# Kernel optimization log

Hardware: AMD Instinct MI355X
Metric: run time of the kernel (lower is better)

The kernel has to match this reference:

```python
import jax, jax.numpy as jnp
import numpy as np

B, N, D, H = 1, 4096, 768, 12
HD = D // H
SCALE = HD ** -0.5

def setup_inputs() -> dict:
    key = jax.random.key(0)
    k1, k2, k3 = jax.random.split(key, 3)
    x = jax.random.normal(k1, (B, N, D), dtype=jnp.float32)
    W_qkv = jax.random.normal(k2, (D, 3 * D), dtype=jnp.float32) * (D ** -0.5)
    W_out = jax.random.normal(k3, (D, D), dtype=jnp.float32) * (D ** -0.5)
    b_out = jnp.zeros((D,), dtype=jnp.float32)
    return {"x": x, "W_qkv": W_qkv, "W_out": W_out, "b_out": b_out}

def reference(x, W_qkv, W_out, b_out):
    # qkv projection: (B,N,3D)
    qkv = x @ W_qkv
    q, k, v = jnp.split(qkv, 3, axis=-1)
    # (B,N,D) -> (B,H,N,hd)
    def heads(t):
        return t.reshape(B, N, H, HD).transpose(0, 2, 1, 3)
    q, k, v = heads(q), heads(k), heads(v)
    scores = jnp.einsum('bhnd,bhmd->bhnm', q, k) * SCALE  # (B,H,N,N)
    attn = jax.nn.softmax(scores, axis=-1)
    out = jnp.einsum('bhnm,bhmd->bhnd', attn, v)
    out = out.transpose(0, 2, 1, 3).reshape(B, N, D)
    return out @ W_out + b_out
```

## Files before the change

kernel.cpp:

```cpp
#include <hip/hip_runtime.h>
#include <hip/hip_bf16.h>
#include <math.h>

typedef __attribute__((ext_vector_type(8))) short bf16x8;
typedef __attribute__((ext_vector_type(4))) float floatx4;

constexpr int kN  = 4096;
constexpr int kD  = 768;
constexpr int kH  = 12;
constexpr int kHD = 64;
constexpr int k3D = 2304;
constexpr float kQScale = 0.18033688011112042f;

static __device__ __forceinline__ short f2b(float f) {
    __hip_bfloat16 h = __float2bfloat16(f);
    return *reinterpret_cast<short*>(&h);
}

static __device__ __forceinline__ float fast_exp2(float x) {
#if __has_builtin(__builtin_amdgcn_exp2f)
    return __builtin_amdgcn_exp2f(x);
#else
    return exp2f(x);
#endif
}

static __device__ __forceinline__ void async_copy16(const void* g, void* l) {
    __builtin_amdgcn_global_load_lds(
        (const __attribute__((address_space(1))) void*)g,
        (__attribute__((address_space(3))) void*)l, 16, 0, 0);
}

__global__ __launch_bounds__(256)
void convX(const float* __restrict__ src, short* __restrict__ dst, int n8)
{
    int i = blockIdx.x * 256 + threadIdx.x;
    if (i < n8) {
        const float4* s = reinterpret_cast<const float4*>(src + (size_t)i * 8);
        float4 a = s[0], b = s[1];
        bf16x8 v;
        v[0] = f2b(a.x); v[1] = f2b(a.y); v[2] = f2b(a.z); v[3] = f2b(a.w);
        v[4] = f2b(b.x); v[5] = f2b(b.y); v[6] = f2b(b.z); v[7] = f2b(b.w);
        *reinterpret_cast<bf16x8*>(dst + (size_t)i * 8) = v;
    }
}

__global__ void convT(const float* __restrict__ src, short* __restrict__ dst,
                      int R, int C)
{
    __shared__ float t[32][33];
    const int c0 = blockIdx.x * 32, r0 = blockIdx.y * 32;
    const int tx = threadIdx.x, ty = threadIdx.y;
    #pragma unroll
    for (int i = ty; i < 32; i += 8)
        t[i][tx] = src[(size_t)(r0 + i) * C + c0 + tx];
    __syncthreads();
    #pragma unroll
    for (int i = ty; i < 32; i += 8)
        dst[(size_t)(c0 + i) * R + r0 + tx] = f2b(t[tx][i]);
}

__global__ __launch_bounds__(256)
void gemm_bt(const short* __restrict__ A, const short* __restrict__ BT,
             const float* __restrict__ bias, float* __restrict__ Cout,
             short* __restrict__ Qh, short* __restrict__ Kh, short* __restrict__ Vt,
             int N, int K, int mode)
{
    const int bm   = blockIdx.x * 128;
    const int bn   = blockIdx.y * 128;
    const int tid  = threadIdx.x;
    const int wave = tid >> 6;
    const int lane = tid & 63;
    const int l15  = lane & 15;
    const int quad = lane >> 4;
    const int l3   = l15 & 3;

    __shared__ alignas(16) short As[128 * 32];
    __shared__ alignas(16) short Bs[128 * 32];

    floatx4 acc[4][4] = {};
    const int wm = (wave >> 1) * 64;
    const int wn = (wave & 1) * 64;

    const int srl = lane >> 2;
    const int scc = (lane & 3) ^ (srl & 3);

    for (int k0 = 0; k0 < K; k0 += 32) {
        __syncthreads();
        #pragma unroll
        for (int j = 0; j < 2; ++j) {
            const int rs = 32 * wave + 16 * j;
            async_copy16(&A [(size_t)(bm + rs + srl) * K + k0 + 8 * scc], &As[rs * 32]);
            async_copy16(&BT[(size_t)(bn + rs + srl) * K + k0 + 8 * scc], &Bs[rs * 32]);
        }
        __syncthreads();

        bf16x8 af[4], bfr[4];
        #pragma unroll
        for (int mt = 0; mt < 4; ++mt)
            af[mt] = *reinterpret_cast<const bf16x8*>(&As[(wm + 16 * mt + l15) * 32 + 8 * (quad ^ l3)]);
        #pragma unroll
        for (int nt = 0; nt < 4; ++nt)
            bfr[nt] = *reinterpret_cast<const bf16x8*>(&Bs[(wn + 16 * nt + l15) * 32 + 8 * (quad ^ l3)]);
        #pragma unroll
        for (int mt = 0; mt < 4; ++mt)
            #pragma unroll
            for (int nt = 0; nt < 4; ++nt)
                acc[mt][nt] = __builtin_amdgcn_mfma_f32_16x16x32_bf16(af[mt], bfr[nt], acc[mt][nt], 0, 0, 0);
    }

    #pragma unroll
    for (int mt = 0; mt < 4; ++mt) {
        #pragma unroll
        for (int nt = 0; nt < 4; ++nt) {
            #pragma unroll
            for (int r = 0; r < 4; ++r) {
                const int row = bm + wm + mt * 16 + 4 * quad + r;
                const int col = bn + wn + nt * 16 + l15;
                float v = acc[mt][nt][r];
                if (mode == 0) {
                    Cout[(size_t)row * N + col] = v + bias[col];
                } else {
                    const int proj   = col / kD;
                    const int within = col - proj * kD;
                    const int h = within >> 6;
                    const int d = within & 63;
                    if (proj == 0)      Qh[((size_t)h * kN + row) * kHD + d] = f2b(v * kQScale);
                    else if (proj == 1) Kh[((size_t)h * kN + row) * kHD + d] = f2b(v);
                    else                Vt[((size_t)h * kHD + d) * kN + row] = f2b(v);
                }
            }
        }
    }
}

__global__ __launch_bounds__(256)
void attn(const short* __restrict__ Qh, const short* __restrict__ Kh,
          const short* __restrict__ Vt, short* __restrict__ AO)
{
    const int h    = blockIdx.y;
    const int q0   = blockIdx.x * 64;
    const int tid  = threadIdx.x;
    const int wave = tid >> 6;
    const int lane = tid & 63;
    const int l15  = lane & 15;
    const int quad = lane >> 4;
    const int lx   = l15 & 7;

    __shared__ alignas(16) short Ks[128 * 64];
    __shared__ alignas(16) short Vs[64 * 128];

    const int qrow = q0 + 16 * wave + l15;
    const size_t qbase = ((size_t)h * kN + qrow) * kHD;
    bf16x8 qf[2];
    qf[0] = *reinterpret_cast<const bf16x8*>(&Qh[qbase + quad * 8]);
    qf[1] = *reinterpret_cast<const bf16x8*>(&Qh[qbase + 32 + quad * 8]);

    floatx4 oacc[4] = {};
    float psum[4] = {0.f, 0.f, 0.f, 0.f};

    const int krl = lane >> 3;
    const int kcc = (lane & 7) ^ (krl & 7);
    const int vrl = lane >> 4;
    const int vp  = lane & 15;

    short* Pw = Ks + wave * 2048;

    for (int kv0 = 0; kv0 < kN; kv0 += 128) {
        __syncthreads();
        #pragma unroll
        for (int j = 0; j < 4; ++j) {
            const int rk = 32 * wave + 8 * j;
            async_copy16(&Kh[((size_t)h * kN + kv0 + rk + krl) * kHD + 8 * kcc],
                         &Ks[rk * 64]);
            const int rv0 = 16 * wave + 4 * j;
            const int rv  = rv0 + vrl;
            async_copy16(&Vt[((size_t)h * kHD + rv) * kN + kv0 + 8 * (vp ^ (rv & 7))],
                         &Vs[rv0 * 128]);
        }
        __syncthreads();

        floatx4 sacc[8] = {};
        #pragma unroll
        for (int nt = 0; nt < 8; ++nt) {
            #pragma unroll
            for (int s = 0; s < 2; ++s) {
                bf16x8 kf = *reinterpret_cast<const bf16x8*>(
                    &Ks[(16 * nt + l15) * 64 + 8 * ((4 * s + quad) ^ lx)]);
                sacc[nt] = __builtin_amdgcn_mfma_f32_16x16x32_bf16(qf[s], kf, sacc[nt], 0, 0, 0);
            }
        }
        __syncthreads();

        #pragma unroll
        for (int nt = 0; nt < 8; ++nt) {
            #pragma unroll
            for (int r = 0; r < 4; ++r) {
                const float p = fast_exp2(sacc[nt][r]);
                const int m = 4 * quad + r;
                Pw[m * 128 + 8 * ((2 * nt + (l15 >> 3)) ^ (m & 7)) + (l15 & 7)] = f2b(p);
                psum[r] += p;
            }
        }

        #pragma unroll
        for (int s = 0; s < 4; ++s) {
            bf16x8 pa = *reinterpret_cast<const bf16x8*>(
                &Pw[l15 * 128 + 8 * ((4 * s + quad) ^ lx)]);
            #pragma unroll
            for (int dt = 0; dt < 4; ++dt) {
                bf16x8 vv = *reinterpret_cast<const bf16x8*>(
                    &Vs[(16 * dt + l15) * 128 + 8 * ((4 * s + quad) ^ lx)]);
                oacc[dt] = __builtin_amdgcn_mfma_f32_16x16x32_bf16(pa, vv, oacc[dt], 0, 0, 0);
            }
        }
    }

    float lrow[4];
    #pragma unroll
    for (int r = 0; r < 4; ++r) {
        float v = psum[r];
        #pragma unroll
        for (int off = 8; off >= 1; off >>= 1)
            v += __shfl_xor(v, off);
        lrow[r] = v;
    }

    #pragma unroll
    for (int dt = 0; dt < 4; ++dt) {
        #pragma unroll
        for (int r = 0; r < 4; ++r) {
            const int row = q0 + 16 * wave + 4 * quad + r;
            const int col = h * kHD + 16 * dt + l15;
            AO[(size_t)row * kD + col] = f2b(oacc[dt][r] / lrow[r]);
        }
    }
}

extern "C" void kernel_launch(void* const* d_in, const int* in_sizes, int n_in,
                              void* d_out, int out_size, void* d_ws, size_t ws_size,
                              hipStream_t stream)
{
    const float* x     = (const float*)d_in[0];
    const float* W_qkv = (const float*)d_in[1];
    const float* W_out = (const float*)d_in[2];
    const float* b_out = (const float*)d_in[3];
    float* out = (float*)d_out;

    const size_t HNHD = (size_t)kH * kN * kHD;
    short* Qh    = (short*)d_ws;
    short* Kh    = Qh + HNHD;
    short* Vt    = Kh + HNHD;
    short* Xb    = Vt + HNHD;
    short* WqkvT = Xb + (size_t)kN * kD;
    short* WoutT = WqkvT + (size_t)k3D * kD;
    short* AO    = Xb;
    (void)in_sizes; (void)n_in; (void)out_size; (void)ws_size;

    convX<<<dim3((kN * kD / 8 + 255) / 256), dim3(256), 0, stream>>>(x, Xb, kN * kD / 8);
    convT<<<dim3(k3D / 32, kD / 32), dim3(32, 8), 0, stream>>>(W_qkv, WqkvT, kD, k3D);
    convT<<<dim3(kD / 32, kD / 32), dim3(32, 8), 0, stream>>>(W_out, WoutT, kD, kD);

    gemm_bt<<<dim3(kN / 128, k3D / 128), dim3(256), 0, stream>>>(
        Xb, WqkvT, nullptr, nullptr, Qh, Kh, Vt, k3D, kD, 1);
    attn<<<dim3(kN / 64, kH), dim3(256), 0, stream>>>(Qh, Kh, Vt, AO);
    gemm_bt<<<dim3(kN / 128, kD / 128), dim3(256), 0, stream>>>(
        AO, WoutT, b_out, out, nullptr, nullptr, nullptr, kD, kD, 0);
}
```

Before: 227.9 us.

## Merge prep kernels, template GEMM modes, and reswizzle attention P buffer

Folds the X conversion and both weight transposes into one prep launch, which removes two kernel launches. The GEMM mode becomes a template parameter so each specialization drops its runtime branch in the epilogue. In attention, the P tile's XOR swizzle changes from m&7 to (5*m)&15 and the write loop is reordered so the row base is computed once, aiming to cut LDS bank conflicts on the P writes and reads. The new swizzle must stay consistent between the write and read sides or the results will be wrong.

```diff
diff --git a/kernel.cpp b/kernel.cpp
--- a/kernel.cpp
+++ b/kernel.cpp
@@ -31,26 +31,38 @@
         (__attribute__((address_space(3))) void*)l, 16, 0, 0);
 }
 
-__global__ __launch_bounds__(256)
-void convX(const float* __restrict__ src, short* __restrict__ dst, int n8)
-{
-    int i = blockIdx.x * 256 + threadIdx.x;
-    if (i < n8) {
-        const float4* s = reinterpret_cast<const float4*>(src + (size_t)i * 8);
+constexpr int kBlkX  = 1536;
+constexpr int kBlkWq = 72 * 24;
+constexpr int kBlkWo = 24 * 24;
+
+__global__ __launch_bounds__(256)
+void prep(const float* __restrict__ x, const float* __restrict__ Wq,
+          const float* __restrict__ Wo, short* __restrict__ Xb,
+          short* __restrict__ WqT, short* __restrict__ WoT)
+{
+    const int bid = blockIdx.x;
+    const int tid = threadIdx.x;
+    if (bid < kBlkX) {
+        const int i = bid * 256 + tid;
+        const float4* s = reinterpret_cast<const float4*>(x + (size_t)i * 8);
         float4 a = s[0], b = s[1];
         bf16x8 v;
         v[0] = f2b(a.x); v[1] = f2b(a.y); v[2] = f2b(a.z); v[3] = f2b(a.w);
         v[4] = f2b(b.x); v[5] = f2b(b.y); v[6] = f2b(b.z); v[7] = f2b(b.w);
-        *reinterpret_cast<bf16x8*>(dst + (size_t)i * 8) = v;
-    }
-}
-
-__global__ void convT(const float* __restrict__ src, short* __restrict__ dst,
-                      int R, int C)
-{
+        *reinterpret_cast<bf16x8*>(Xb + (size_t)i * 8) = v;
+        return;
+    }
+    const float* src; short* dst; int R, C, bx, by;
+    if (bid < kBlkX + kBlkWq) {
+        const int local = bid - kBlkX;
+        src = Wq; dst = WqT; R = kD; C = k3D; bx = local % 72; by = local / 72;
+    } else {
+        const int local = bid - kBlkX - kBlkWq;
+        src = Wo; dst = WoT; R = kD; C = kD; bx = local % 24; by = local / 24;
+    }
     __shared__ float t[32][33];
-    const int c0 = blockIdx.x * 32, r0 = blockIdx.y * 32;
-    const int tx = threadIdx.x, ty = threadIdx.y;
+    const int c0 = bx * 32, r0 = by * 32;
+    const int tx = tid & 31, ty = tid >> 5;
     #pragma unroll
     for (int i = ty; i < 32; i += 8)
         t[i][tx] = src[(size_t)(r0 + i) * C + c0 + tx];
@@ -60,11 +72,12 @@
         dst[(size_t)(c0 + i) * R + r0 + tx] = f2b(t[tx][i]);
 }
 
-__global__ __launch_bounds__(256)
-void gemm_bt(const short* __restrict__ A, const short* __restrict__ BT,
-             const float* __restrict__ bias, float* __restrict__ Cout,
-             short* __restrict__ Qh, short* __restrict__ Kh, short* __restrict__ Vt,
-             int N, int K, int mode)
+template<int MODE>
+__device__ __forceinline__
+void gemm_core(const short* __restrict__ A, const short* __restrict__ BT,
+               const float* __restrict__ bias, float* __restrict__ Cout,
+               short* __restrict__ Qh, short* __restrict__ Kh, short* __restrict__ Vt,
+               int N, int K)
 {
     const int bm   = blockIdx.x * 128;
     const int bn   = blockIdx.y * 128;
@@ -118,7 +131,7 @@
                 const int row = bm + wm + mt * 16 + 4 * quad + r;
                 const int col = bn + wn + nt * 16 + l15;
                 float v = acc[mt][nt][r];
-                if (mode == 0) {
+                if (MODE == 0) {
                     Cout[(size_t)row * N + col] = v + bias[col];
                 } else {
                     const int proj   = col / kD;
@@ -135,6 +148,20 @@
 }
 
 __global__ __launch_bounds__(256)
+void gemm_qkv(const short* __restrict__ A, const short* __restrict__ BT,
+              short* __restrict__ Qh, short* __restrict__ Kh, short* __restrict__ Vt)
+{
+    gemm_core<1>(A, BT, nullptr, nullptr, Qh, Kh, Vt, k3D, kD);
+}
+
+__global__ __launch_bounds__(256)
+void gemm_out(const short* __restrict__ A, const short* __restrict__ BT,
+              const float* __restrict__ bias, float* __restrict__ Cout)
+{
+    gemm_core<0>(A, BT, bias, Cout, nullptr, nullptr, nullptr, kD, kD);
+}
+
+__global__ __launch_bounds__(256)
 void attn(const short* __restrict__ Qh, const short* __restrict__ Kh,
           const short* __restrict__ Vt, short* __restrict__ AO)
 {
@@ -165,6 +192,7 @@
     const int vp  = lane & 15;
 
     short* Pw = Ks + wave * 2048;
+    const int rmask = (5 * l15) & 15;
 
     for (int kv0 = 0; kv0 < kN; kv0 += 128) {
         __syncthreads();
@@ -193,12 +221,14 @@
         __syncthreads();
 
         #pragma unroll
-        for (int nt = 0; nt < 8; ++nt) {
-            #pragma unroll
-            for (int r = 0; r < 4; ++r) {
+        for (int r = 0; r < 4; ++r) {
+            const int m = 4 * quad + r;
+            const int wmask = (5 * m) & 15;
+            short* prow = Pw + m * 128 + (l15 & 7);
+            #pragma unroll
+            for (int nt = 0; nt < 8; ++nt) {
                 const float p = fast_exp2(sacc[nt][r]);
-                const int m = 4 * quad + r;
-                Pw[m * 128 + 8 * ((2 * nt + (l15 >> 3)) ^ (m & 7)) + (l15 & 7)] = f2b(p);
+                prow[8 * ((2 * nt + (l15 >> 3)) ^ wmask)] = f2b(p);
                 psum[r] += p;
             }
         }
@@ -206,7 +236,7 @@
         #pragma unroll
         for (int s = 0; s < 4; ++s) {
             bf16x8 pa = *reinterpret_cast<const bf16x8*>(
-                &Pw[l15 * 128 + 8 * ((4 * s + quad) ^ lx)]);
+                &Pw[l15 * 128 + 8 * ((4 * s + quad) ^ rmask)]);
             #pragma unroll
             for (int dt = 0; dt < 4; ++dt) {
                 bf16x8 vv = *reinterpret_cast<const bf16x8*>(
@@ -257,13 +287,12 @@
     short* AO    = Xb;
     (void)in_sizes; (void)n_in; (void)out_size; (void)ws_size;
 
-    convX<<<dim3((kN * kD / 8 + 255) / 256), dim3(256), 0, stream>>>(x, Xb, kN * kD / 8);
-    convT<<<dim3(k3D / 32, kD / 32), dim3(32, 8), 0, stream>>>(W_qkv, WqkvT, kD, k3D);
-    convT<<<dim3(kD / 32, kD / 32), dim3(32, 8), 0, stream>>>(W_out, WoutT, kD, kD);
-
-    gemm_bt<<<dim3(kN / 128, k3D / 128), dim3(256), 0, stream>>>(
-        Xb, WqkvT, nullptr, nullptr, Qh, Kh, Vt, k3D, kD, 1);
+    prep<<<dim3(kBlkX + kBlkWq + kBlkWo), dim3(256), 0, stream>>>(
+        x, W_qkv, W_out, Xb, WqkvT, WoutT);
+
+    gemm_qkv<<<dim3(kN / 128, k3D / 128), dim3(256), 0, stream>>>(
+        Xb, WqkvT, Qh, Kh, Vt);
     attn<<<dim3(kN / 64, kH), dim3(256), 0, stream>>>(Qh, Kh, Vt, AO);
-    gemm_bt<<<dim3(kN / 128, kD / 128), dim3(256), 0, stream>>>(
-        AO, WoutT, b_out, out, nullptr, nullptr, nullptr, kD, kD, 0);
-}
+    gemm_out<<<dim3(kN / 128, kD / 128), dim3(256), 0, stream>>>(
+        AO, WoutT, b_out, out);
+}
```

New measurement: 212.6 us. -6.7%, faster.
